# Optimization experiments

Measured on AMD Instinct MI355X. Metric: run time of the kernel, lower is better.

Reference implementation:

```python
import jax, jax.numpy as jnp
import numpy as np

N_NODES = 10000
N_EDGES = 160000
C_IN = 64      # in_irreps = 64x0e
C_TP = 16      # in_tp_irreps = 16x0e
C_KEY = 8      # key_irreps = (mul//2) = 8x0e
C_SH = 4       # spherical_harmonics_irreps = 4x0e
C_OTP = 16     # out_tp_irreps = 16x0e
C_OUT = 64     # out_irreps = 64x0e
EF = 32        # n_edge_features
FC = 128       # fc_dim (hardcoded in module)
W_NUMEL_K = C_TP * C_SH * C_KEY   # 512
W_NUMEL_V = C_TP * C_SH * C_OTP   # 1024
EPS = 1e-5


def _mlp(x, W1, b1, W2, b2, W3, b3):
    h = jax.nn.relu(x @ W1 + b1)
    h = jax.nn.relu(h @ W2 + b2)
    return h @ W3 + b3


def setup_inputs() -> dict:
    key = jax.random.key(0)
    ks = jax.random.split(key, 24)
    def nrm(k, shape, scale=1.0):
        return jax.random.normal(k, shape, dtype=jnp.float32) * scale
    inp = {}
    inp["node_data"] = nrm(ks[0], (N_NODES, C_IN))
    inp["edge_index"] = jax.random.randint(ks[1], (2, N_EDGES), 0, N_NODES, dtype=jnp.int32)
    inp["edge_data"] = nrm(ks[2], (N_EDGES, EF))
    inp["edge_sh"] = nrm(ks[3], (N_EDGES, C_SH))
    # e3nn Linear / TP internal weights (scalar-irrep specialization)
    inp["W_input"] = nrm(ks[4], (C_IN, C_TP))
    inp["W_query"] = nrm(ks[5], (C_TP, C_KEY))
    inp["W_dot"] = nrm(ks[6], (C_KEY, C_KEY))
    inp["W_output"] = nrm(ks[7], (C_OTP, C_OUT))
    # fc_key MLP: EF -> FC -> FC -> W_NUMEL_K
    inp["Wk1"] = nrm(ks[8], (EF, FC), 1.0 / np.sqrt(EF)); inp["bk1"] = jnp.zeros((FC,), jnp.float32)
    inp["Wk2"] = nrm(ks[9], (FC, FC), 1.0 / np.sqrt(FC)); inp["bk2"] = jnp.zeros((FC,), jnp.float32)
    inp["Wk3"] = nrm(ks[10], (FC, W_NUMEL_K), 1.0 / np.sqrt(FC)); inp["bk3"] = jnp.zeros((W_NUMEL_K,), jnp.float32)
    # fc_value MLP: EF -> FC -> FC -> W_NUMEL_V
    inp["Wv1"] = nrm(ks[11], (EF, FC), 1.0 / np.sqrt(EF)); inp["bv1"] = jnp.zeros((FC,), jnp.float32)
    inp["Wv2"] = nrm(ks[12], (FC, FC), 1.0 / np.sqrt(FC)); inp["bv2"] = jnp.zeros((FC,), jnp.float32)
    inp["Wv3"] = nrm(ks[13], (FC, W_NUMEL_V), 1.0 / np.sqrt(FC)); inp["bv3"] = jnp.zeros((W_NUMEL_V,), jnp.float32)
    inp["bn_weight"] = jnp.ones((C_OUT,), jnp.float32)
    inp["bn_bias"] = jnp.zeros((C_OUT,), jnp.float32)
    return inp


def reference(node_data, edge_index, edge_data, edge_sh,
              W_input, W_query, W_dot, W_output,
              Wk1, bk1, Wk2, bk2, Wk3, bk3,
              Wv1, bv1, Wv2, bv2, Wv3, bv3,
              bn_weight, bn_bias):
    N = node_data.shape[0]
    E = edge_data.shape[0]
    src, dst = edge_index[0], edge_index[1]

    # input_linear (e3nn Linear -> fan-in normalized matmul for scalar irreps)
    t = node_data @ W_input / np.sqrt(C_IN)          # [N, C_TP]
    q = t @ W_query / np.sqrt(C_TP)                  # [N, C_KEY]

    # dynamically generated per-edge TP weights
    wk = _mlp(edge_data, Wk1, bk1, Wk2, bk2, Wk3, bk3).reshape(E, C_TP, C_SH, C_KEY)
    wv = _mlp(edge_data, Wv1, bv1, Wv2, bv2, Wv3, bv3).reshape(E, C_TP, C_SH, C_OTP)

    ts = t[src]                                      # gather source node features [E, C_TP]
    # FullyConnectedTensorProduct on scalar irreps == per-edge weighted bilinear
    k = jnp.einsum('ea,es,easb->eb', ts, edge_sh, wk) / np.sqrt(C_TP * C_SH)   # [E, C_KEY]
    v = jnp.einsum('ea,es,easb->eb', ts, edge_sh, wv) / np.sqrt(C_TP * C_SH)   # [E, C_OTP]

    # dot(q[dest], k) -> scalar attention logit per edge
    a = (jnp.einsum('ea,eb,ab->e', q[dst], k, W_dot) / np.sqrt(C_KEY * C_KEY))[:, None]  # [E, 1]

    # segment softmax over edges grouped by destination node
    m = jax.ops.segment_max(a, dst, num_segments=N)
    m = jnp.where(jnp.isfinite(m), m, 0.0)           # empty segments -> 0 (matches scatter_max fill)
    a = jnp.exp(a - m[dst])
    z = jax.ops.segment_sum(a, dst, num_segments=N)
    a = a / z[dst]

    agg = jax.ops.segment_sum(a * v, dst, num_segments=N)   # [N, C_OTP]

    out = agg @ W_output / np.sqrt(C_OTP)            # [N, C_OUT]
    # residual: F.pad(node_data, (0, C_OUT - C_IN)); here C_OUT == C_IN so plain add
    out = out + node_data

    # e3nn BatchNorm on scalar irreps (training-mode batch stats, affine)
    mean = out.mean(axis=0)
    c = out - mean
    var = (c * c).mean(axis=0)
    out = c * jax.lax.rsqrt(var + EPS) * bn_weight + bn_bias
    return out
```

## Files before the change

kernel.cpp:

```cpp
#include <hip/hip_runtime.h>

#define N_NODES 10000
#define N_EDGES 160000

typedef unsigned short u16;
typedef unsigned int   u32;
typedef __bf16 bf16x8 __attribute__((ext_vector_type(8)));
typedef float  f32x4  __attribute__((ext_vector_type(4)));
typedef unsigned short u16x4 __attribute__((ext_vector_type(4)));

struct InP { const void* p[22]; };

static constexpr size_t WS_FLAG = 0;
static constexpr size_t WS_WIN  = 256;
static constexpr size_t WS_WQ   = WS_WIN  + 4096;
static constexpr size_t WS_WD   = WS_WQ   + 512;
static constexpr size_t WS_WOUT = WS_WD   + 256;
static constexpr size_t WS_BK1  = WS_WOUT + 4096;
static constexpr size_t WS_BK2  = WS_BK1  + 512;
static constexpr size_t WS_BK3  = WS_BK2  + 512;
static constexpr size_t WS_BV1  = WS_BK3  + 2048;
static constexpr size_t WS_BV2  = WS_BV1  + 512;
static constexpr size_t WS_BV3  = WS_BV2  + 512;
static constexpr size_t WS_BNW  = WS_BV3  + 4096;
static constexpr size_t WS_BNB  = WS_BNW  + 256;
static constexpr size_t WS_WK1T = WS_BNB  + 256;
static constexpr size_t WS_WK2T = WS_WK1T + 8192;
static constexpr size_t WS_WK3T = WS_WK2T + 32768;
static constexpr size_t WS_WV1T = WS_WK3T + 131072;
static constexpr size_t WS_WV2T = WS_WV1T + 8192;
static constexpr size_t WS_WV3T = WS_WV2T + 32768;
static constexpr size_t WS_T    = WS_WV3T + 262144;
static constexpr size_t WS_Q    = WS_T    + (size_t)N_NODES*16*4;
static constexpr size_t WS_Z    = WS_Q    + (size_t)N_NODES*8*4;
static constexpr size_t WS_AGG  = WS_Z    + (size_t)N_NODES*4;
static constexpr size_t WS_BNS  = WS_AGG  + (size_t)N_NODES*16*4;
static constexpr size_t WS_BNQ  = WS_BNS  + 256;
static constexpr size_t WS_OUTP = WS_BNQ  + 256;
static constexpr size_t ZERO_OFF = WS_Z;
static constexpr size_t ZERO_LEN = WS_OUTP - WS_Z;

__device__ __forceinline__ float loadf(const void* p, long i, int isbf){
  if(isbf){
    u32 x = ((u32)((const u16*)p)[i]) << 16;
    return __uint_as_float(x);
  }
  return ((const float*)p)[i];
}
__device__ __forceinline__ u16 f2b(float f){
  u32 u = __float_as_uint(f);
  u += 0x7fffu + ((u >> 16) & 1u);
  return (u16)(u >> 16);
}
__device__ __forceinline__ float b2f(u16 v){
  return __uint_as_float(((u32)v) << 16);
}
__device__ __forceinline__ bf16x8 ld8(const u16* p){
  uint4 v = *(const uint4*)p;
  return __builtin_bit_cast(bf16x8, v);
}

__global__ void k_detect(const void* edge_data, int* flag){
  int lane = threadIdx.x;
  u16 v = ((const u16*)edge_data)[lane*2];
  int ex = (v >> 7) & 0xFF;
  int sane = (ex >= 100 && ex <= 140) ? 1 : 0;
  unsigned long long b = __ballot(sane);
  if(lane == 0) flag[0] = (__popcll(b) >= 48) ? 1 : 0;
}

__global__ void k_convert(InP in, char* ws){
  const int isbf = *(const int*)(ws + WS_FLAG);
  long idx = (long)blockIdx.x*256 + threadIdx.x;
  const int    fsrc[12] = {4,5,6,7,9,11,13,15,17,19,20,21};
  const int    fcnt[12] = {1024,128,64,1024,128,128,512,128,128,1024,64,64};
  const size_t fdst[12] = {WS_WIN,WS_WQ,WS_WD,WS_WOUT,WS_BK1,WS_BK2,WS_BK3,WS_BV1,WS_BV2,WS_BV3,WS_BNW,WS_BNB};
  const long F_TOTAL = 4416;
  if(idx < F_TOTAL){
    long g = idx;
    for(int s=0;s<12;s++){
      if(g < fcnt[s]){ ((float*)(ws+fdst[s]))[g] = loadf(in.p[fsrc[s]], g, isbf); return; }
      g -= fcnt[s];
    }
    return;
  }
  long g = idx - F_TOTAL;
  const int    tsrc[6] = {8,10,12,14,16,18};
  const int    tK[6]   = {32,128,128,32,128,128};
  const int    tN[6]   = {128,128,512,128,128,1024};
  const size_t tdst[6] = {WS_WK1T,WS_WK2T,WS_WK3T,WS_WV1T,WS_WV2T,WS_WV3T};
  for(int s=0;s<6;s++){
    long cnt = (long)tK[s]*tN[s];
    if(g < cnt){
      int nk = tK[s] >> 5;
      int i = (int)(g & 7), ln = (int)((g>>3) & 63);
      int r2 = (int)(g >> 9);
      int kk = r2 % nk; int r3 = r2 / nk;
      int nt = r3 & 1;  int c  = r3 >> 1;
      int n = c*32 + nt*16 + (ln & 15);
      int k = kk*32 + (ln >> 4)*8 + i;
      ((u16*)(ws+tdst[s]))[g] = f2b(loadf(in.p[tsrc[s]], (long)k*tN[s] + n, isbf));
      return;
    }
    g -= cnt;
  }
}

__global__ void k_tq(InP in, char* ws){
  const int isbf = *(const int*)(ws + WS_FLAG);
  __shared__ float sWin[1024];
  __shared__ float sWq[128];
  __shared__ float sN[1024];
  __shared__ float sT[256];
  float* t_ws = (float*)(ws+WS_T);
  float* q_ws = (float*)(ws+WS_Q);
  int tid = threadIdx.x;
  for(int i=tid;i<1024;i+=256) sWin[i] = ((const float*)(ws+WS_WIN))[i];
  if(tid<128) sWq[tid] = ((const float*)(ws+WS_WQ))[tid];
  int n0 = blockIdx.x*16;
  for(int i=tid;i<1024;i+=256) sN[i] = loadf(in.p[0], (long)n0*64 + i, isbf);
  __syncthreads();
  int ni = tid>>4, j = tid&15;
  float acc = 0.f;
  #pragma unroll 8
  for(int i=0;i<64;i++) acc += sN[ni*64+i]*sWin[i*16+j];
  float t = acc*0.125f;
  t_ws[(n0+ni)*16+j] = t;
  sT[tid] = t;
  __syncthreads();
  if(tid<128){
    int n2 = tid>>3, b = tid&7;
    float a2 = 0.f;
    #pragma unroll
    for(int jj=0;jj<16;jj++) a2 += sT[n2*16+jj]*sWq[jj*8+b];
    q_ws[(n0+n2)*8+b] = a2*0.25f;
  }
}


__device__ __forceinline__ void dense1(int wv, int lane, int lquad, int lrow,
                                       const u16* __restrict__ Wg,
                                       const float* __restrict__ biasg,
                                       const u16* sED, u16* sH1){
  bf16x8 bw0 = ld8(&Wg[((wv*2+0)<<9) + lane*8]);
  bf16x8 bw1 = ld8(&Wg[((wv*2+1)<<9) + lane*8]);
  f32x4 bb0 = *(const f32x4*)&biasg[wv*32 +  0 + lquad*4];
  f32x4 bb1 = *(const f32x4*)&biasg[wv*32 + 16 + lquad*4];
  #pragma unroll
  for(int et=0;et<4;et++){
    bf16x8 a = ld8(&sED[et*512 + lane*8]);
    f32x4 c0 = __builtin_amdgcn_mfma_f32_16x16x32_bf16(bw0, a, bb0, 0, 0, 0);
    f32x4 c1 = __builtin_amdgcn_mfma_f32_16x16x32_bf16(bw1, a, bb1, 0, 0, 0);
    u16x4 pk0, pk1;
    #pragma unroll
    for(int r=0;r<4;r++){
      float h0 = c0[r] > 0.f ? c0[r] : 0.f; pk0[r] = f2b(h0);
      float h1 = c1[r] > 0.f ? c1[r] : 0.f; pk1[r] = f2b(h1);
    }
    int base = et*2048 + (wv<<9) + (lquad>>1)*128 + lrow*8 + (lquad&1)*4;
    *(u16x4*)&sH1[base      ] = pk0;
    *(u16x4*)&sH1[base + 256] = pk1;
  }
}

template<int NC, int ISVAL>
__device__ __forceinline__ void l23(int wv, int lane, int lquad, int lrow,
                                    const u16* __restrict__ W2, const float* __restrict__ b2,
                                    const u16* __restrict__ W3, const float* __restrict__ b3,
                                    const u16* sH1, const u16* sPT, float* sKV){
  const int hi = lane >> 5;
  const int s0 = ((lane>>4)&1)*32 + (lane&15);

  bf16x8 w20 = ld8(&W2[(((wv*2+0)*4+0)<<9) + lane*8]);
  bf16x8 w21 = ld8(&W2[(((wv*2+0)*4+1)<<9) + lane*8]);
  bf16x8 w22 = ld8(&W2[(((wv*2+0)*4+2)<<9) + lane*8]);
  bf16x8 w23 = ld8(&W2[(((wv*2+0)*4+3)<<9) + lane*8]);
  bf16x8 w24 = ld8(&W2[(((wv*2+1)*4+0)<<9) + lane*8]);
  bf16x8 w25 = ld8(&W2[(((wv*2+1)*4+1)<<9) + lane*8]);
  bf16x8 w26 = ld8(&W2[(((wv*2+1)*4+2)<<9) + lane*8]);
  bf16x8 w27 = ld8(&W2[(((wv*2+1)*4+3)<<9) + lane*8]);
  f32x4 bb20 = *(const f32x4*)&b2[wv*32 +  0 + lquad*4];
  f32x4 bb21 = *(const f32x4*)&b2[wv*32 + 16 + lquad*4];

  bf16x8 af0, af1, af2, af3;
#define D2_ET(ET, AF) { \
    bf16x8 a0 = ld8(&sH1[ET*2048 + (0<<9) + lane*8]); \
    bf16x8 a1 = ld8(&sH1[ET*2048 + (1<<9) + lane*8]); \
    bf16x8 a2 = ld8(&sH1[ET*2048 + (2<<9) + lane*8]); \
    bf16x8 a3 = ld8(&sH1[ET*2048 + (3<<9) + lane*8]); \
    f32x4 c0 = bb20, c1 = bb21; \
    c0 = __builtin_amdgcn_mfma_f32_16x16x32_bf16(w20, a0, c0, 0, 0, 0); \
    c0 = __builtin_amdgcn_mfma_f32_16x16x32_bf16(w21, a1, c0, 0, 0, 0); \
    c0 = __builtin_amdgcn_mfma_f32_16x16x32_bf16(w22, a2, c0, 0, 0, 0); \
    c0 = __builtin_amdgcn_mfma_f32_16x16x32_bf16(w23, a3, c0, 0, 0, 0); \
    c1 = __builtin_amdgcn_mfma_f32_16x16x32_bf16(w24, a0, c1, 0, 0, 0); \
    c1 = __builtin_amdgcn_mfma_f32_16x16x32_bf16(w25, a1, c1, 0, 0, 0); \
    c1 = __builtin_amdgcn_mfma_f32_16x16x32_bf16(w26, a2, c1, 0, 0, 0); \
    c1 = __builtin_amdgcn_mfma_f32_16x16x32_bf16(w27, a3, c1, 0, 0, 0); \
    float h0 = c0[0]>0.f?c0[0]:0.f, h1 = c0[1]>0.f?c0[1]:0.f; \
    float h2 = c0[2]>0.f?c0[2]:0.f, h3 = c0[3]>0.f?c0[3]:0.f; \
    u32 p00 = ((u32)f2b(h1)<<16) | (u32)f2b(h0); \
    u32 p01 = ((u32)f2b(h3)<<16) | (u32)f2b(h2); \
    h0 = c1[0]>0.f?c1[0]:0.f; h1 = c1[1]>0.f?c1[1]:0.f; \
    h2 = c1[2]>0.f?c1[2]:0.f; h3 = c1[3]>0.f?c1[3]:0.f; \
    u32 p10 = ((u32)f2b(h1)<<16) | (u32)f2b(h0); \
    u32 p11 = ((u32)f2b(h3)<<16) | (u32)f2b(h2); \
    int a00 = __shfl((int)p00, s0),    a01 = __shfl((int)p01, s0); \
    int a10 = __shfl((int)p10, s0),    a11 = __shfl((int)p11, s0); \
    int b00 = __shfl((int)p00, s0+16), b01 = __shfl((int)p01, s0+16); \
    int b10 = __shfl((int)p10, s0+16), b11 = __shfl((int)p11, s0+16); \
    uint4 uv; \
    uv.x = (u32)(hi ? a10 : a00); \
    uv.y = (u32)(hi ? a11 : a01); \
    uv.z = (u32)(hi ? b10 : b00); \
    uv.w = (u32)(hi ? b11 : b01); \
    AF = __builtin_bit_cast(bf16x8, uv); }
  D2_ET(0, af0)
  D2_ET(1, af1)
  D2_ET(2, af2)
  D2_ET(3, af3)
#undef D2_ET

  f32x4 kp0 = {0.f,0.f,0.f,0.f}, kp1 = {0.f,0.f,0.f,0.f};
  f32x4 kp2 = {0.f,0.f,0.f,0.f}, kp3 = {0.f,0.f,0.f,0.f};
#define MV_ET(ET, AF, KP) { \
      const int e = ET*16 + lrow; \
      f32x4 c0 = __builtin_amdgcn_mfma_f32_16x16x32_bf16(w30, AF, bb30, 0, 0, 0); \
      f32x4 c1 = __builtin_amdgcn_mfma_f32_16x16x32_bf16(w31, AF, bb31, 0, 0, 0); \
      const int n00 = j*32 +  0 + lquad*4; \
      const int n01 = j*32 + 16 + lquad*4; \
      const int as0 = ISVAL ? (n00>>4) : (n00>>3); \
      const int as1 = ISVAL ? (n01>>4) : (n01>>3); \
      const float pv0 = b2f(sPT[as0*64 + e]); \
      const float pv1 = b2f(sPT[as1*64 + e]); \
      KP += c0*pv0 + c1*pv1; }
  #pragma unroll 2
  for(int j=0;j<NC;j++){
    bf16x8 w30 = ld8(&W3[(((j*2+0)*4 + wv)<<9) + lane*8]);
    bf16x8 w31 = ld8(&W3[(((j*2+1)*4 + wv)<<9) + lane*8]);
    f32x4 bb30 = {0.f,0.f,0.f,0.f}, bb31 = {0.f,0.f,0.f,0.f};
    if(wv == 0){
      bb30 = *(const f32x4*)&b3[j*32 +  0 + lquad*4];
      bb31 = *(const f32x4*)&b3[j*32 + 16 + lquad*4];
    }
    MV_ET(0, af0, kp0)
    MV_ET(1, af1, kp1)
    MV_ET(2, af2, kp2)
    MV_ET(3, af3, kp3)
  }
#undef MV_ET

  const int b0     = ISVAL ? (lquad*4) : ((lquad&1)*4);
  const int stride = ISVAL ? 16 : 8;
#define ST_ET(ET, KP) { \
    const int e = ET*16 + lrow; \
    atomicAdd(&sKV[e*stride + b0 + 0], KP[0]*0.125f); \
    atomicAdd(&sKV[e*stride + b0 + 1], KP[1]*0.125f); \
    atomicAdd(&sKV[e*stride + b0 + 2], KP[2]*0.125f); \
    atomicAdd(&sKV[e*stride + b0 + 3], KP[3]*0.125f); }
  ST_ET(0, kp0)
  ST_ET(1, kp1)
  ST_ET(2, kp2)
  ST_ET(3, kp3)
#undef ST_ET
}

__global__ __launch_bounds__(256,3) void k_edges(InP in, char* ws){
  const int isbf = *(const int*)(ws + WS_FLAG);
  const int* ei = (const int*)in.p[1];
  const float* t_ws = (const float*)(ws + WS_T);
  const float* q_ws = (const float*)(ws + WS_Q);
  float* Zp  = (float*)(ws + WS_Z);
  float* AGG = (float*)(ws + WS_AGG);

  __shared__ __align__(16) char smem[34816];
  u16*   sED = (u16*)smem;
  u16*   sH1 = (u16*)(smem + 4096);
  u16*   sPT = (u16*)(smem + 20480);
  float* sK  = (float*)(smem + 28672);
  float* sV  = (float*)(smem + 30720);
  float* sP  = (float*)smem;
  int*   sDst= (int*)(smem + 256);

  const int tid  = threadIdx.x;
  const int e0   = blockIdx.x * 64;
  const int lane = tid & 63, wv = tid >> 6;
  const int lrow = lane & 15, lquad = lane >> 4;

  {
    int e = tid >> 2, q4 = tid & 3;
    u16 tmp[8];
    if(isbf){
      uint4 vv = *(const uint4*)((const u16*)in.p[2] + (long)(e0+e)*32 + q4*8);
      *(uint4*)tmp = vv;
    } else {
      const float* fp = (const float*)in.p[2] + (long)(e0+e)*32 + q4*8;
      f32x4 a = *(const f32x4*)fp, b = *(const f32x4*)(fp+4);
      #pragma unroll
      for(int r=0;r<4;r++){ tmp[r]=f2b(a[r]); tmp[4+r]=f2b(b[r]); }
    }
    *(uint4*)&sED[(e>>4)*512 + (q4*16 + (e&15))*8] = *(uint4*)tmp;
  }
  {
    int e = tid >> 2, j4 = tid & 3;
    int src = ei[e0+e];
    *(f32x4*)&sV[e*16 + j4*4] = *(const f32x4*)&t_ws[src*16 + j4*4];
  }
  {
    int e = tid >> 2, s4 = tid & 3;
    sK[tid] = loadf(in.p[3], (long)(e0+e)*4 + s4, isbf);
  }
  float qreg[8]; int mydst = 0;
  if(wv == 0){
    mydst = ei[N_EDGES + e0 + lane];
    #pragma unroll
    for(int a=0;a<8;a++) qreg[a] = q_ws[mydst*8 + a];
  }
  __syncthreads();
  for(int idx = tid; idx < 4096; idx += 256){
    int e = idx & 63, as = idx >> 6;
    sPT[as*64 + e] = f2b(sV[e*16 + (as>>2)] * sK[e*4 + (as&3)]);
  }
  __syncthreads();
  for(int idx = tid; idx < 1536; idx += 256) sK[idx] = 0.f;

  dense1(wv, lane, lquad, lrow, (const u16*)(ws+WS_WK1T), (const float*)(ws+WS_BK1), sED, sH1);
  __syncthreads();
  l23<16,0>(wv, lane, lquad, lrow,
            (const u16*)(ws+WS_WK2T), (const float*)(ws+WS_BK2),
            (const u16*)(ws+WS_WK3T), (const float*)(ws+WS_BK3), sH1, sPT, sK);
  __syncthreads();
  dense1(wv, lane, lquad, lrow, (const u16*)(ws+WS_WV1T), (const float*)(ws+WS_BV1), sED, sH1);
  __syncthreads();
  l23<32,1>(wv, lane, lquad, lrow,
            (const u16*)(ws+WS_WV2T), (const float*)(ws+WS_BV2),
            (const u16*)(ws+WS_WV3T), (const float*)(ws+WS_BV3), sH1, sPT, sV);
  __syncthreads();

  if(wv == 0){
    const float* wdf = (const float*)(ws + WS_WD);
    float acc = 0.f;
    #pragma unroll
    for(int a=0;a<8;a++){
      float qa = qreg[a];
      #pragma unroll
      for(int b=0;b<8;b++)
        acc += qa * wdf[a*8+b] * sK[lane*8+b];
    }
    float p = __expf(acc * 0.125f);
    atomicAdd(Zp + mydst, p);
    sP[lane] = p;
    sDst[lane] = mydst;
  }
  __syncthreads();
  for(int idx = tid; idx < 1024; idx += 256){
    int e = idx >> 4;
    atomicAdd(AGG + (long)sDst[e]*16 + (idx & 15), sP[e]*sV[idx]);
  }
}

__global__ void k7a(InP in, char* ws){
  const int isbf = *(const int*)(ws + WS_FLAG);
  __shared__ float sWo[1024];
  __shared__ float ls[256], lq[256];
  int tid = threadIdx.x;
  for(int i=tid;i<1024;i+=256) sWo[i] = ((const float*)(ws+WS_WOUT))[i];
  __syncthreads();
  const float* AGG = (const float*)(ws+WS_AGG);
  const float* Zp  = (const float*)(ws+WS_Z);
  float* OUTP = (float*)(ws+WS_OUTP);
  int c = tid & 63, r4 = tid >> 6;
  float s=0.f, q=0.f;
  for(int it=0; it<20; it++){
    int n = blockIdx.x*80 + it*4 + r4;
    float z = Zp[n];
    float inv = z > 0.f ? 0.25f/z : 0.f;
    const float* ag = AGG + (long)n*16;
    float acc = 0.f;
    #pragma unroll
    for(int j=0;j<16;j++) acc += ag[j]*sWo[j*64+c];
    float o = acc*inv + loadf(in.p[0], (long)n*64 + c, isbf);
    OUTP[(long)n*64+c] = o;
    s += o; q += o*o;
  }
  ls[tid]=s; lq[tid]=q;
  __syncthreads();
  if(tid < 64){
    float ss = ls[tid]+ls[tid+64]+ls[tid+128]+ls[tid+192];
    float qq = lq[tid]+lq[tid+64]+lq[tid+128]+lq[tid+192];
    atomicAdd((float*)(ws+WS_BNS)+tid, ss);
    atomicAdd((float*)(ws+WS_BNQ)+tid, qq);
  }
}

__global__ void k7c(char* ws, void* d_out){
  const int isbf = *(const int*)(ws + WS_FLAG);
  int idx = blockIdx.x*256 + threadIdx.x;
  if(idx >= N_NODES*64) return;
  int c = idx & 63;
  float s  = ((const float*)(ws+WS_BNS))[c];
  float qq = ((const float*)(ws+WS_BNQ))[c];
  float mean = s * (1.f/N_NODES);
  float var  = qq * (1.f/N_NODES) - mean*mean;
  float sc = rsqrtf(var + 1e-5f) * ((const float*)(ws+WS_BNW))[c];
  float val = (((const float*)(ws+WS_OUTP))[idx] - mean)*sc + ((const float*)(ws+WS_BNB))[c];
  if(isbf) ((u16*)d_out)[idx] = f2b(val);
  else     ((float*)d_out)[idx] = val;
}

extern "C" void kernel_launch(void* const* d_in, const int* in_sizes, int n_in,
                              void* d_out, int out_size, void* d_ws, size_t ws_size,
                              hipStream_t stream){
  InP in;
  for(int i=0;i<22;i++) in.p[i] = d_in[i];
  char* ws = (char*)d_ws;

  hipMemsetAsync(ws + ZERO_OFF, 0, ZERO_LEN, stream);
  k_detect<<<1,64,0,stream>>>((const void*)d_in[2], (int*)(ws+WS_FLAG));
  k_convert<<<946,256,0,stream>>>(in, ws);
  k_tq<<<625,256,0,stream>>>(in, ws);
  k_edges<<<2500,256,0,stream>>>(in, ws);
  k7a<<<125,256,0,stream>>>(in, ws);
  k7c<<<2500,256,0,stream>>>(ws, d_out);
}
```

Measured before the change: 328.1 us.

## Load edge features into registers, spread attention logit over all waves

Edge features are now loaded straight into MFMA operand registers in the fragment layout, which removes the sED shared-memory staging buffer and shrinks LDS from 34816 to 30720 bytes. The attention-logit dot product, previously done by wave 0 alone after both MLPs, is now split across all four waves with cross-lane shuffle reductions and computed between the key and value passes. bf16 packing uses native __bf16 conversions (pk2) instead of manual rounding, and the sPT transpose writes two values per store. Edge features are kept live in registers across both dense1 calls, which raises register pressure under launch_bounds(256,3).

```diff
diff --git a/kernel.cpp b/kernel.cpp
--- a/kernel.cpp
+++ b/kernel.cpp
@@ -5,6 +5,7 @@
 
 typedef unsigned short u16;
 typedef unsigned int   u32;
+typedef __bf16 bf16x2 __attribute__((ext_vector_type(2)));
 typedef __bf16 bf16x8 __attribute__((ext_vector_type(8)));
 typedef float  f32x4  __attribute__((ext_vector_type(4)));
 typedef unsigned short u16x4 __attribute__((ext_vector_type(4)));
@@ -59,6 +60,13 @@
   uint4 v = *(const uint4*)p;
   return __builtin_bit_cast(bf16x8, v);
 }
+__device__ __forceinline__ u32 pk2(float lo, float hi){
+  bf16x2 v;
+  v[0] = (__bf16)lo;
+  v[1] = (__bf16)hi;
+  return __builtin_bit_cast(u32, v);
+}
+__device__ __forceinline__ float relu(float x){ return x > 0.f ? x : 0.f; }
 
 __global__ void k_detect(const void* edge_data, int* flag){
   int lane = threadIdx.x;
@@ -141,26 +149,26 @@
 __device__ __forceinline__ void dense1(int wv, int lane, int lquad, int lrow,
                                        const u16* __restrict__ Wg,
                                        const float* __restrict__ biasg,
-                                       const u16* sED, u16* sH1){
+                                       bf16x8 d0, bf16x8 d1, bf16x8 d2, bf16x8 d3,
+                                       u16* sH1){
   bf16x8 bw0 = ld8(&Wg[((wv*2+0)<<9) + lane*8]);
   bf16x8 bw1 = ld8(&Wg[((wv*2+1)<<9) + lane*8]);
   f32x4 bb0 = *(const f32x4*)&biasg[wv*32 +  0 + lquad*4];
   f32x4 bb1 = *(const f32x4*)&biasg[wv*32 + 16 + lquad*4];
-  #pragma unroll
-  for(int et=0;et<4;et++){
-    bf16x8 a = ld8(&sED[et*512 + lane*8]);
-    f32x4 c0 = __builtin_amdgcn_mfma_f32_16x16x32_bf16(bw0, a, bb0, 0, 0, 0);
-    f32x4 c1 = __builtin_amdgcn_mfma_f32_16x16x32_bf16(bw1, a, bb1, 0, 0, 0);
-    u16x4 pk0, pk1;
-    #pragma unroll
-    for(int r=0;r<4;r++){
-      float h0 = c0[r] > 0.f ? c0[r] : 0.f; pk0[r] = f2b(h0);
-      float h1 = c1[r] > 0.f ? c1[r] : 0.f; pk1[r] = f2b(h1);
-    }
-    int base = et*2048 + (wv<<9) + (lquad>>1)*128 + lrow*8 + (lquad&1)*4;
-    *(u16x4*)&sH1[base      ] = pk0;
-    *(u16x4*)&sH1[base + 256] = pk1;
-  }
+#define D1_ET(ET, D) { \
+    f32x4 c0 = __builtin_amdgcn_mfma_f32_16x16x32_bf16(bw0, D, bb0, 0, 0, 0); \
+    f32x4 c1 = __builtin_amdgcn_mfma_f32_16x16x32_bf16(bw1, D, bb1, 0, 0, 0); \
+    int base = ET*2048 + (wv<<9) + (lquad>>1)*128 + lrow*8 + (lquad&1)*4; \
+    uint2 u0, u1; \
+    u0.x = pk2(relu(c0[0]), relu(c0[1])); u0.y = pk2(relu(c0[2]), relu(c0[3])); \
+    u1.x = pk2(relu(c1[0]), relu(c1[1])); u1.y = pk2(relu(c1[2]), relu(c1[3])); \
+    *(uint2*)&sH1[base      ] = u0; \
+    *(uint2*)&sH1[base + 256] = u1; }
+  D1_ET(0, d0)
+  D1_ET(1, d1)
+  D1_ET(2, d2)
+  D1_ET(3, d3)
+#undef D1_ET
 }
 
 template<int NC, int ISVAL>
@@ -197,14 +205,10 @@
     c1 = __builtin_amdgcn_mfma_f32_16x16x32_bf16(w25, a1, c1, 0, 0, 0); \
     c1 = __builtin_amdgcn_mfma_f32_16x16x32_bf16(w26, a2, c1, 0, 0, 0); \
     c1 = __builtin_amdgcn_mfma_f32_16x16x32_bf16(w27, a3, c1, 0, 0, 0); \
-    float h0 = c0[0]>0.f?c0[0]:0.f, h1 = c0[1]>0.f?c0[1]:0.f; \
-    float h2 = c0[2]>0.f?c0[2]:0.f, h3 = c0[3]>0.f?c0[3]:0.f; \
-    u32 p00 = ((u32)f2b(h1)<<16) | (u32)f2b(h0); \
-    u32 p01 = ((u32)f2b(h3)<<16) | (u32)f2b(h2); \
-    h0 = c1[0]>0.f?c1[0]:0.f; h1 = c1[1]>0.f?c1[1]:0.f; \
-    h2 = c1[2]>0.f?c1[2]:0.f; h3 = c1[3]>0.f?c1[3]:0.f; \
-    u32 p10 = ((u32)f2b(h1)<<16) | (u32)f2b(h0); \
-    u32 p11 = ((u32)f2b(h3)<<16) | (u32)f2b(h2); \
+    u32 p00 = pk2(relu(c0[0]), relu(c0[1])); \
+    u32 p01 = pk2(relu(c0[2]), relu(c0[3])); \
+    u32 p10 = pk2(relu(c1[0]), relu(c1[1])); \
+    u32 p11 = pk2(relu(c1[2]), relu(c1[3])); \
     int a00 = __shfl((int)p00, s0),    a01 = __shfl((int)p01, s0); \
     int a10 = __shfl((int)p10, s0),    a11 = __shfl((int)p11, s0); \
     int b00 = __shfl((int)p00, s0+16), b01 = __shfl((int)p01, s0+16); \
@@ -273,12 +277,11 @@
   float* Zp  = (float*)(ws + WS_Z);
   float* AGG = (float*)(ws + WS_AGG);
 
-  __shared__ __align__(16) char smem[34816];
-  u16*   sED = (u16*)smem;
-  u16*   sH1 = (u16*)(smem + 4096);
-  u16*   sPT = (u16*)(smem + 20480);
-  float* sK  = (float*)(smem + 28672);
-  float* sV  = (float*)(smem + 30720);
+  __shared__ __align__(16) char smem[30720];
+  u16*   sH1 = (u16*)smem;
+  u16*   sPT = (u16*)(smem + 16384);
+  float* sK  = (float*)(smem + 24576);
+  float* sV  = (float*)(smem + 26624);
   float* sP  = (float*)smem;
   int*   sDst= (int*)(smem + 256);
 
@@ -287,20 +290,24 @@
   const int lane = tid & 63, wv = tid >> 6;
   const int lrow = lane & 15, lquad = lane >> 4;
 
-  {
-    int e = tid >> 2, q4 = tid & 3;
-    u16 tmp[8];
-    if(isbf){
-      uint4 vv = *(const uint4*)((const u16*)in.p[2] + (long)(e0+e)*32 + q4*8);
-      *(uint4*)tmp = vv;
-    } else {
-      const float* fp = (const float*)in.p[2] + (long)(e0+e)*32 + q4*8;
-      f32x4 a = *(const f32x4*)fp, b = *(const f32x4*)(fp+4);
-      #pragma unroll
-      for(int r=0;r<4;r++){ tmp[r]=f2b(a[r]); tmp[4+r]=f2b(b[r]); }
-    }
-    *(uint4*)&sED[(e>>4)*512 + (q4*16 + (e&15))*8] = *(uint4*)tmp;
-  }
+  bf16x8 ed0, ed1, ed2, ed3;
+#define LOAD_ED(ET, ED) { \
+    long row = (long)(e0 + ET*16 + lrow); \
+    if(isbf){ \
+      ED = ld8((const u16*)in.p[2] + row*32 + lquad*8); \
+    } else { \
+      const float* fp = (const float*)in.p[2] + row*32 + lquad*8; \
+      f32x4 a = *(const f32x4*)fp, b = *(const f32x4*)(fp+4); \
+      uint4 uv; \
+      uv.x = pk2(a[0],a[1]); uv.y = pk2(a[2],a[3]); \
+      uv.z = pk2(b[0],b[1]); uv.w = pk2(b[2],b[3]); \
+      ED = __builtin_bit_cast(bf16x8, uv); } }
+  LOAD_ED(0, ed0)
+  LOAD_ED(1, ed1)
+  LOAD_ED(2, ed2)
+  LOAD_ED(3, ed3)
+#undef LOAD_ED
+
   {
     int e = tid >> 2, j4 = tid & 3;
     int src = ei[e0+e];
@@ -310,47 +317,60 @@
     int e = tid >> 2, s4 = tid & 3;
     sK[tid] = loadf(in.p[3], (long)(e0+e)*4 + s4, isbf);
   }
-  float qreg[8]; int mydst = 0;
-  if(wv == 0){
-    mydst = ei[N_EDGES + e0 + lane];
-    #pragma unroll
-    for(int a=0;a<8;a++) qreg[a] = q_ws[mydst*8 + a];
-  }
-  __syncthreads();
-  for(int idx = tid; idx < 4096; idx += 256){
-    int e = idx & 63, as = idx >> 6;
-    sPT[as*64 + e] = f2b(sV[e*16 + (as>>2)] * sK[e*4 + (as&3)]);
+  const int eL = wv*16 + lrow;
+  int mydst = ei[N_EDGES + e0 + eL];
+  float qa = q_ws[mydst*8 + lquad];
+  float qb = q_ws[mydst*8 + 4 + lquad];
+  __syncthreads();
+  for(int idx = tid; idx < 2048; idx += 256){
+    int as = idx >> 5, ep = (idx & 31)*2;
+    float v0 = sV[ep*16     + (as>>2)] * sK[ep*4     + (as&3)];
+    float v1 = sV[(ep+1)*16 + (as>>2)] * sK[(ep+1)*4 + (as&3)];
+    ((u32*)sPT)[as*32 + (idx&31)] = pk2(v0, v1);
   }
   __syncthreads();
   for(int idx = tid; idx < 1536; idx += 256) sK[idx] = 0.f;
 
-  dense1(wv, lane, lquad, lrow, (const u16*)(ws+WS_WK1T), (const float*)(ws+WS_BK1), sED, sH1);
+  dense1(wv, lane, lquad, lrow, (const u16*)(ws+WS_WK1T), (const float*)(ws+WS_BK1),
+         ed0, ed1, ed2, ed3, sH1);
   __syncthreads();
   l23<16,0>(wv, lane, lquad, lrow,
             (const u16*)(ws+WS_WK2T), (const float*)(ws+WS_BK2),
             (const u16*)(ws+WS_WK3T), (const float*)(ws+WS_BK3), sH1, sPT, sK);
   __syncthreads();
-  dense1(wv, lane, lquad, lrow, (const u16*)(ws+WS_WV1T), (const float*)(ws+WS_BV1), sED, sH1);
+
+  float p;
+  {
+    const float* wdf = (const float*)(ws + WS_WD);
+    f32x4 wa0 = *(const f32x4*)&wdf[lquad*8];
+    f32x4 wa1 = *(const f32x4*)&wdf[lquad*8 + 4];
+    f32x4 wb0 = *(const f32x4*)&wdf[(4+lquad)*8];
+    f32x4 wb1 = *(const f32x4*)&wdf[(4+lquad)*8 + 4];
+    f32x4 k0 = *(const f32x4*)&sK[eL*8];
+    f32x4 k1 = *(const f32x4*)&sK[eL*8 + 4];
+    float part = 0.f;
+    #pragma unroll
+    for(int r=0;r<4;r++){
+      part += (qa*wa0[r] + qb*wb0[r]) * k0[r];
+      part += (qa*wa1[r] + qb*wb1[r]) * k1[r];
+    }
+    part += __shfl_xor(part, 16);
+    part += __shfl_xor(part, 32);
+    p = __expf(part * 0.125f);
+  }
+
+  dense1(wv, lane, lquad, lrow, (const u16*)(ws+WS_WV1T), (const float*)(ws+WS_BV1),
+         ed0, ed1, ed2, ed3, sH1);
   __syncthreads();
   l23<32,1>(wv, lane, lquad, lrow,
             (const u16*)(ws+WS_WV2T), (const float*)(ws+WS_BV2),
             (const u16*)(ws+WS_WV3T), (const float*)(ws+WS_BV3), sH1, sPT, sV);
   __syncthreads();
 
-  if(wv == 0){
-    const float* wdf = (const float*)(ws + WS_WD);
-    float acc = 0.f;
-    #pragma unroll
-    for(int a=0;a<8;a++){
-      float qa = qreg[a];
-      #pragma unroll
-      for(int b=0;b<8;b++)
-        acc += qa * wdf[a*8+b] * sK[lane*8+b];
-    }
-    float p = __expf(acc * 0.125f);
+  if(lquad == 0){
     atomicAdd(Zp + mydst, p);
-    sP[lane] = p;
-    sDst[lane] = mydst;
+    sP[eL] = p;
+    sDst[eL] = mydst;
   }
   __syncthreads();
   for(int idx = tid; idx < 1024; idx += 256){
@@ -415,7 +435,7 @@
   for(int i=0;i<22;i++) in.p[i] = d_in[i];
   char* ws = (char*)d_ws;
 
-  hipMemsetAsync(ws + ZERO_OFF, 0, ZERO_LEN, stream);
+  (void)hipMemsetAsync(ws + ZERO_OFF, 0, ZERO_LEN, stream);
   k_detect<<<1,64,0,stream>>>((const void*)d_in[2], (int*)(ws+WS_FLAG));
   k_convert<<<946,256,0,stream>>>(in, ws);
   k_tq<<<625,256,0,stream>>>(in, ws);
```

After: 336.0 us. 2.4% more time.
